# Kernel optimization log

Hardware: AMD Instinct MI355X
Metric: run time of the kernel (lower is better)

## Reference

```python
import jax, jax.numpy as jnp
import numpy as np
import math

B, H, T, DH, D = 1, 8, 2048, 64, 64
NEG_INF = -1e30
EPS = 1e-9

def setup_inputs() -> dict:
    key = jax.random.key(0)
    ks = jax.random.split(key, 6)
    q = jax.random.normal(ks[0], (B, H, T, DH), dtype=jnp.float32)
    k = jax.random.normal(ks[1], (B, H, T, DH), dtype=jnp.float32)
    v = jax.random.normal(ks[2], (B, H, T, DH), dtype=jnp.float32)
    edge_type_bias = 0.1 * jax.random.normal(ks[3], (4,), dtype=jnp.float32)
    neigh_idx = jax.random.randint(ks[4], (H, T, D), 0, T).astype(jnp.int32)
    edge_type = jax.random.randint(ks[5], (H, T, D), 0, 5).astype(jnp.int32)
    return {"q": q, "k": k, "v": v, "edge_type_bias": edge_type_bias,
            "neigh_idx": neigh_idx, "edge_type": edge_type}

def _masked_softmax(scores, mask):
    # scores: [B,H,T,D] fp32, mask: [1,H,T,D] bool; zeros on all-masked rows
    masked = jnp.where(mask, scores, NEG_INF)
    m = jnp.max(masked, axis=-1, keepdims=True)
    e = jnp.where(mask, jnp.exp(masked - m), 0.0)
    denom = jnp.maximum(jnp.sum(e, axis=-1, keepdims=True), EPS)
    return e / denom

def reference(q, k, v, edge_type_bias, neigh_idx, edge_type):
    Bq, Hq, Tq, dh = q.shape
    # safe_neighbor_idx: clamp to valid range
    s_idx = jnp.clip(neigh_idx, 0, Tq - 1)                       # [H,T,D]
    # causal_neighbor_mask: valid (>=0) and neighbor <= query position
    pos = jnp.arange(Tq, dtype=neigh_idx.dtype)[None, :, None]    # [1,T,1]
    mask = (neigh_idx >= 0) & (neigh_idx <= pos)                  # [H,T,D]
    # edge-type bias: type 0 -> no bias, types 1..4 -> learnable bias
    full_bias = jnp.concatenate([jnp.zeros((1,), jnp.float32),
                                 edge_type_bias.astype(jnp.float32)])
    bias_htd = full_bias[edge_type]                               # [H,T,D]
    # gather neighbor K/V: k_g[b,h,t,n,:] = k[b,h,s_idx[h,t,n],:]
    h_ix = jnp.arange(Hq)[:, None, None]                          # [H,1,1]
    k_g = k[:, h_ix, s_idx]                                       # [B,H,T,D,dh]
    v_g = v[:, h_ix, s_idx]                                       # [B,H,T,D,dh]
    scores = jnp.einsum('bhtc,bhtnc->bhtn',
                        q.astype(jnp.float32),
                        k_g.astype(jnp.float32)) / math.sqrt(dh)
    scores = scores + bias_htd[None]                              # [B,H,T,D]
    w = _masked_softmax(scores, mask[None])                       # [B,H,T,D]
    y = jnp.einsum('bhtn,bhtnc->bhtc', w, v_g.astype(jnp.float32))
    return y.astype(v.dtype)
```

## Files before the change

kernel.cpp:

```cpp
#include <hip/hip_runtime.h>
#include <hip/hip_fp16.h>

constexpr int H  = 8;
constexpr int T  = 2048;
constexpr int DH = 64;
constexpr int D  = 64;
constexpr int NKV = H * T * DH;

typedef _Float16 half2v __attribute__((ext_vector_type(2)));

#if defined(__has_builtin)
#if __has_builtin(__builtin_amdgcn_fdot2)
#define HAVE_FDOT2 1
#endif
#if __has_builtin(__builtin_amdgcn_permlane32_swap)
#define HAVE_PL32 1
#endif
#if __has_builtin(__builtin_amdgcn_permlane16_swap)
#define HAVE_PL16 1
#endif
#endif

__device__ __forceinline__ float dot2acc(half2v a, half2v b, float c) {
#ifdef HAVE_FDOT2
    return __builtin_amdgcn_fdot2(a, b, c, false);
#else
    return c + (float)a.x * (float)b.x + (float)a.y * (float)b.y;
#endif
}

__device__ __forceinline__ half2v h2bits(int b) { return __builtin_bit_cast(half2v, b); }

__device__ __forceinline__ half2v f2h2(float x, float y) {
    __half2 h = __float22half2_rn(make_float2(x, y));
    return __builtin_bit_cast(half2v, h);
}

template<int CTRL>
__device__ __forceinline__ float dpp_mov_f(float x) {
    int yi = __builtin_amdgcn_update_dpp(0, __builtin_bit_cast(int, x),
                                         CTRL, 0xF, 0xF, true);
    return __builtin_bit_cast(float, yi);
}
template<int CTRL>
__device__ __forceinline__ float dpp_add_f(float x) { return x + dpp_mov_f<CTRL>(x); }
template<int CTRL>
__device__ __forceinline__ float dpp_max_f(float x) { return fmaxf(x, dpp_mov_f<CTRL>(x)); }

__device__ __forceinline__ float xor32add_f(float x) {
#ifdef HAVE_PL32
    unsigned u = __builtin_bit_cast(unsigned, x);
    auto r = __builtin_amdgcn_permlane32_swap(u, u, false, false);
    return __builtin_bit_cast(float, (unsigned)r[0]) + __builtin_bit_cast(float, (unsigned)r[1]);
#else
    return x + __shfl_xor(x, 32);
#endif
}
__device__ __forceinline__ float xor32max_f(float x) {
#ifdef HAVE_PL32
    unsigned u = __builtin_bit_cast(unsigned, x);
    auto r = __builtin_amdgcn_permlane32_swap(u, u, false, false);
    return fmaxf(__builtin_bit_cast(float, (unsigned)r[0]), __builtin_bit_cast(float, (unsigned)r[1]));
#else
    return fmaxf(x, __shfl_xor(x, 32));
#endif
}
__device__ __forceinline__ float xor16add_f(float x) {
#ifdef HAVE_PL16
    unsigned u = __builtin_bit_cast(unsigned, x);
    auto r = __builtin_amdgcn_permlane16_swap(u, u, false, false);
    return __builtin_bit_cast(float, (unsigned)r[0]) + __builtin_bit_cast(float, (unsigned)r[1]);
#else
    return x + __shfl_xor(x, 16);
#endif
}
__device__ __forceinline__ float xor16max_f(float x) {
#ifdef HAVE_PL16
    unsigned u = __builtin_bit_cast(unsigned, x);
    auto r = __builtin_amdgcn_permlane16_swap(u, u, false, false);
    return fmaxf(__builtin_bit_cast(float, (unsigned)r[0]), __builtin_bit_cast(float, (unsigned)r[1]));
#else
    return fmaxf(x, __shfl_xor(x, 16));
#endif
}
__device__ __forceinline__ half2v xor32add_h2(half2v x) {
#ifdef HAVE_PL32
    unsigned u = __builtin_bit_cast(unsigned, x);
    auto r = __builtin_amdgcn_permlane32_swap(u, u, false, false);
    return h2bits((int)r[0]) + h2bits((int)r[1]);
#else
    return x + h2bits(__shfl_xor(__builtin_bit_cast(int, x), 32));
#endif
}
__device__ __forceinline__ half2v xor16add_h2(half2v x) {
#ifdef HAVE_PL16
    unsigned u = __builtin_bit_cast(unsigned, x);
    auto r = __builtin_amdgcn_permlane16_swap(u, u, false, false);
    return h2bits((int)r[0]) + h2bits((int)r[1]);
#else
    return x + h2bits(__shfl_xor(__builtin_bit_cast(int, x), 16));
#endif
}
__device__ __forceinline__ half2v xor8add_h2(half2v x) {
    return x + h2bits(__shfl_xor(__builtin_bit_cast(int, x), 8));
}

__global__ __launch_bounds__(256) void cvt_f32_f16(
    const float* __restrict__ k, const float* __restrict__ v,
    __half* __restrict__ kh, __half* __restrict__ vh)
{
    const int i = (blockIdx.x * 256 + threadIdx.x) * 8;
    const float* src = (blockIdx.y == 0) ? k : v;
    __half*      dst = (blockIdx.y == 0) ? kh : vh;
    const float4 a = *reinterpret_cast<const float4*>(src + i);
    const float4 b = *reinterpret_cast<const float4*>(src + i + 4);
    __half2 hh[4];
    hh[0] = __float22half2_rn(make_float2(a.x, a.y));
    hh[1] = __float22half2_rn(make_float2(a.z, a.w));
    hh[2] = __float22half2_rn(make_float2(b.x, b.y));
    hh[3] = __float22half2_rn(make_float2(b.z, b.w));
    *reinterpret_cast<float4*>(dst + i) = *reinterpret_cast<const float4*>(hh);
}

__global__ __launch_bounds__(256) void wayfinder_attn_f16(
    const float* __restrict__ q,
    const __half* __restrict__ kh,
    const __half* __restrict__ vh,
    const float* __restrict__ eb,
    const int*   __restrict__ nidx,
    const int*   __restrict__ etyp,
    float* __restrict__ out)
{
    const int wave = threadIdx.x >> 6;
    const int lane = threadIdx.x & 63;
    const int bid  = blockIdx.x;
    const int work = ((bid & 7) << 9) | (bid >> 3);
    const int flat = (work << 2) + wave;
    const int h    = flat >> 11;
    const int t    = flat & (T - 1);
    const int grp  = lane >> 3;
    const int sub  = lane & 7;

    const long long rowoff = (long long)flat * DH;
    const int*      nrow   = nidx + (long long)flat * D;
    const int*      erow   = etyp + (long long)flat * D;

    const int4 i0 = *reinterpret_cast<const int4*>(nrow + grp * 8);
    const int4 i1 = *reinterpret_cast<const int4*>(nrow + grp * 8 + 4);
    const int4 e0 = *reinterpret_cast<const int4*>(erow + grp * 8);
    const int4 e1 = *reinterpret_cast<const int4*>(erow + grp * 8 + 4);

    const float4 qa = *reinterpret_cast<const float4*>(q + rowoff + sub * 8);
    const float4 qb = *reinterpret_cast<const float4*>(q + rowoff + sub * 8 + 4);

    const int idx_i[8] = {i0.x, i0.y, i0.z, i0.w, i1.x, i1.y, i1.z, i1.w};
    const int et_i [8] = {e0.x, e0.y, e0.z, e0.w, e1.x, e1.y, e1.z, e1.w};

    const __half* khead = kh + (long long)h * T * DH;
    const __half* vhead = vh + (long long)h * T * DH;

    int s_i[8];
    int mskbits = 0;
    #pragma unroll
    for (int i = 0; i < 8; ++i) {
        s_i[i] = min(max(idx_i[i], 0), T - 1);
        mskbits |= ((idx_i[i] >= 0) && (idx_i[i] <= t)) ? (1 << i) : 0;
    }

    float4 kf[8], vf[8];
    #pragma unroll
    for (int i = 0; i < 8; ++i) {
        const long long ro = (long long)s_i[i] * DH + sub * 8;
        kf[i] = *reinterpret_cast<const float4*>(khead + ro);
        vf[i] = *reinterpret_cast<const float4*>(vhead + ro);
    }

    const float4 ebv = *reinterpret_cast<const float4*>(eb);
    float bias_i[8];
    #pragma unroll
    for (int i = 0; i < 8; ++i) {
        const int et = et_i[i];
        bias_i[i] = (et == 1) ? ebv.x : (et == 2) ? ebv.y :
                    (et == 3) ? ebv.z : (et == 4) ? ebv.w : 0.0f;
    }

    half2v qp[4];
    qp[0] = f2h2(qa.x, qa.y);
    qp[1] = f2h2(qa.z, qa.w);
    qp[2] = f2h2(qb.x, qb.y);
    qp[3] = f2h2(qb.z, qb.w);

    float sc[8];
    #pragma unroll
    for (int i = 0; i < 8; ++i) {
        const half2v* kp = reinterpret_cast<const half2v*>(&kf[i]);
        float p = dot2acc(qp[0], kp[0],
                  dot2acc(qp[1], kp[1],
                  dot2acc(qp[2], kp[2],
                  dot2acc(qp[3], kp[3], 0.0f))));
        p = dpp_add_f<0xB1>(p);
        p = dpp_add_f<0x4E>(p);
        p = dpp_add_f<0x141>(p);
        sc[i] = p;
    }

    float masked[8];
    float mx = -1e30f;
    #pragma unroll
    for (int i = 0; i < 8; ++i) {
        const bool mk = (mskbits >> i) & 1;
        masked[i] = mk ? fmaf(sc[i], 0.125f, bias_i[i]) : -1e30f;
        mx = fmaxf(mx, masked[i]);
    }
    mx = dpp_max_f<0x140>(mx);
    mx = xor16max_f(mx);
    mx = xor32max_f(mx);

    float e[8];
    float sum = 0.0f;
    #pragma unroll
    for (int i = 0; i < 8; ++i) {
        const bool mk = (mskbits >> i) & 1;
        e[i] = mk ? __expf(masked[i] - mx) : 0.0f;
        sum += e[i];
    }
    sum = dpp_add_f<0x140>(sum);
    sum = xor16add_f(sum);
    sum = xor32add_f(sum);
    const float rden = 1.0f / fmaxf(sum, 1e-9f);

    float acc[8] = {0.f, 0.f, 0.f, 0.f, 0.f, 0.f, 0.f, 0.f};
    #pragma unroll
    for (int i = 0; i < 8; ++i) {
        const float w = e[i] * rden;
        const half2v* vp = reinterpret_cast<const half2v*>(&vf[i]);
        acc[0] += w * (float)vp[0].x;  acc[1] += w * (float)vp[0].y;
        acc[2] += w * (float)vp[1].x;  acc[3] += w * (float)vp[1].y;
        acc[4] += w * (float)vp[2].x;  acc[5] += w * (float)vp[2].y;
        acc[6] += w * (float)vp[3].x;  acc[7] += w * (float)vp[3].y;
    }

    half2v h0 = f2h2(acc[0], acc[1]);
    half2v h1 = f2h2(acc[2], acc[3]);
    half2v h2 = f2h2(acc[4], acc[5]);
    half2v h3 = f2h2(acc[6], acc[7]);
    h0 = xor8add_h2(h0);  h1 = xor8add_h2(h1);
    h2 = xor8add_h2(h2);  h3 = xor8add_h2(h3);
    h0 = xor16add_h2(h0); h1 = xor16add_h2(h1);
    h2 = xor16add_h2(h2); h3 = xor16add_h2(h3);
    h0 = xor32add_h2(h0); h1 = xor32add_h2(h1);
    h2 = xor32add_h2(h2); h3 = xor32add_h2(h3);

    if (lane < 16) {
        const int s8   = (lane & 7) * 8;
        const int half = lane >> 3;
        const float4 o = half
            ? make_float4((float)h2.x, (float)h2.y, (float)h3.x, (float)h3.y)
            : make_float4((float)h0.x, (float)h0.y, (float)h1.x, (float)h1.y);
        *reinterpret_cast<float4*>(out + rowoff + s8 + half * 4) = o;
    }
}

__global__ __launch_bounds__(256) void wayfinder_attn_f32(
    const float* __restrict__ q, const float* __restrict__ k,
    const float* __restrict__ v, const float* __restrict__ eb,
    const int* __restrict__ nidx, const int* __restrict__ etyp,
    float* __restrict__ out)
{
    const int wave = threadIdx.x >> 6;
    const int lane = threadIdx.x & 63;
    const int flat = (blockIdx.x << 2) + wave;
    const int h    = flat >> 11;
    const int t    = flat & (T - 1);
    const int grp  = lane >> 4;
    const int sub  = lane & 15;

    __shared__ int    sidx[4][64];
    __shared__ float  ssc [4][64];
    __shared__ float2 swv [4][64];

    const long long rowoff = (long long)flat * DH;
    const long long noff = (long long)flat * D + lane;
    const int  idx = nidx[noff];
    const int  et  = etyp[noff];
    const int  s   = min(max(idx, 0), T - 1);
    const bool msk = (idx >= 0) && (idx <= t);
    const float4 ebv  = *reinterpret_cast<const float4*>(eb);
    const float  bias = (et == 1) ? ebv.x : (et == 2) ? ebv.y :
                        (et == 3) ? ebv.z : (et == 4) ? ebv.w : 0.0f;
    sidx[wave][lane] = s;
    const float4 qf = *reinterpret_cast<const float4*>(q + rowoff + sub * 4);
    __syncthreads();

    const float* khead = k + (long long)h * T * DH;
    #pragma unroll
    for (int i = 0; i < 16; ++i) {
        const int n  = i * 4 + grp;
        const int sn = sidx[wave][n];
        const float4 kf = *reinterpret_cast<const float4*>(khead + sn * DH + sub * 4);
        float p = qf.x * kf.x + qf.y * kf.y + qf.z * kf.z + qf.w * kf.w;
        p += __shfl_xor(p, 1);
        p += __shfl_xor(p, 2);
        p += __shfl_xor(p, 4);
        p += __shfl_xor(p, 8);
        if (sub == 0) ssc[wave][n] = p;
    }
    __syncthreads();

    const float sc     = ssc[wave][lane];
    const float masked = msk ? (sc * 0.125f + bias) : -1e30f;
    float mx = masked;
    #pragma unroll
    for (int off = 32; off > 0; off >>= 1) mx = fmaxf(mx, __shfl_xor(mx, off));
    const float e = msk ? __expf(masked - mx) : 0.0f;
    float sum = e;
    #pragma unroll
    for (int off = 32; off > 0; off >>= 1) sum += __shfl_xor(sum, off);
    const float w = e / fmaxf(sum, 1e-9f);
    swv[wave][lane] = make_float2(w, __int_as_float(s));
    __syncthreads();

    const float* vhead = v + (long long)h * T * DH;
    float4 acc = make_float4(0.f, 0.f, 0.f, 0.f);
    #pragma unroll
    for (int i = 0; i < 16; ++i) {
        const int    n  = i * 4 + grp;
        const float2 ws = swv[wave][n];
        const int    sn = __float_as_int(ws.y);
        const float4 vf = *reinterpret_cast<const float4*>(vhead + sn * DH + sub * 4);
        acc.x += ws.x * vf.x; acc.y += ws.x * vf.y;
        acc.z += ws.x * vf.z; acc.w += ws.x * vf.w;
    }
    #pragma unroll
    for (int off = 16; off <= 32; off <<= 1) {
        acc.x += __shfl_xor(acc.x, off); acc.y += __shfl_xor(acc.y, off);
        acc.z += __shfl_xor(acc.z, off); acc.w += __shfl_xor(acc.w, off);
    }
    if (lane < 16)
        *reinterpret_cast<float4*>(out + rowoff + sub * 4) = acc;
}

extern "C" void kernel_launch(void* const* d_in, const int* in_sizes, int n_in,
                              void* d_out, int out_size, void* d_ws, size_t ws_size,
                              hipStream_t stream) {
    const float* q    = (const float*)d_in[0];
    const float* k    = (const float*)d_in[1];
    const float* v    = (const float*)d_in[2];
    const float* eb   = (const float*)d_in[3];
    const int*   nidx = (const int*)d_in[4];
    const int*   etyp = (const int*)d_in[5];
    float* out = (float*)d_out;

    const size_t need = (size_t)2 * NKV * sizeof(__half);
    if (ws_size >= need) {
        __half* kh = (__half*)d_ws;
        __half* vh = kh + NKV;
        dim3 cgrid(NKV / (256 * 8), 2);
        hipLaunchKernelGGL(cvt_f32_f16, cgrid, dim3(256), 0, stream, k, v, kh, vh);
        hipLaunchKernelGGL(wayfinder_attn_f16, dim3(H * T / 4), dim3(256), 0, stream,
                           q, kh, vh, eb, nidx, etyp, out);
    } else {
        hipLaunchKernelGGL(wayfinder_attn_f32, dim3(H * T / 4), dim3(256), 0, stream,
                           q, k, v, eb, nidx, etyp, out);
    }
}
```

Measured before the change: 25.32 us.

## Compact causally-valid neighbors via ballot and skip gathers of masked entries

Each wave loads its 64 neighbor indices one per lane, ballots the causal mask, and compacts the valid indices and edge types into a shared-memory buffer using mbcnt prefix positions. The K/V gather, the dot products and the V accumulation then run only for as many 8-wide chunks as there are valid neighbors, which skips memory traffic for masked neighbors (on average about half, given the causal mask on random indices). In exchange it adds an LDS round trip and wave-uniform branching. It also relies on an intra-wave LDS write-then-read with no explicit barrier.

```diff
diff --git a/kernel.cpp b/kernel.cpp
--- a/kernel.cpp
+++ b/kernel.cpp
@@ -18,6 +18,9 @@
 #endif
 #if __has_builtin(__builtin_amdgcn_permlane16_swap)
 #define HAVE_PL16 1
+#endif
+#if __has_builtin(__builtin_amdgcn_mbcnt_lo)
+#define HAVE_MBCNT 1
 #endif
 #endif
 
@@ -131,6 +134,8 @@
     const int*   __restrict__ etyp,
     float* __restrict__ out)
 {
+    __shared__ int cbuf[4][64];
+
     const int wave = threadIdx.x >> 6;
     const int lane = threadIdx.x & 63;
     const int bid  = blockIdx.x;
@@ -142,47 +147,26 @@
     const int sub  = lane & 7;
 
     const long long rowoff = (long long)flat * DH;
-    const int*      nrow   = nidx + (long long)flat * D;
-    const int*      erow   = etyp + (long long)flat * D;
-
-    const int4 i0 = *reinterpret_cast<const int4*>(nrow + grp * 8);
-    const int4 i1 = *reinterpret_cast<const int4*>(nrow + grp * 8 + 4);
-    const int4 e0 = *reinterpret_cast<const int4*>(erow + grp * 8);
-    const int4 e1 = *reinterpret_cast<const int4*>(erow + grp * 8 + 4);
+
+    const int idx = nidx[(long long)flat * D + lane];
+    const int et  = etyp[(long long)flat * D + lane];
+    const bool mk = (unsigned)idx <= (unsigned)t;
+
+    const unsigned long long M = __ballot(mk);
+    const int total = __builtin_amdgcn_readfirstlane((int)__popcll(M));
+#ifdef HAVE_MBCNT
+    const int pos = __builtin_amdgcn_mbcnt_hi((unsigned)(M >> 32),
+                    __builtin_amdgcn_mbcnt_lo((unsigned)M, 0u));
+#else
+    const int pos = (int)__popcll(M & ((1ull << lane) - 1ull));
+#endif
+    if (mk) cbuf[wave][pos] = idx | (et << 11);
 
     const float4 qa = *reinterpret_cast<const float4*>(q + rowoff + sub * 8);
     const float4 qb = *reinterpret_cast<const float4*>(q + rowoff + sub * 8 + 4);
 
-    const int idx_i[8] = {i0.x, i0.y, i0.z, i0.w, i1.x, i1.y, i1.z, i1.w};
-    const int et_i [8] = {e0.x, e0.y, e0.z, e0.w, e1.x, e1.y, e1.z, e1.w};
-
     const __half* khead = kh + (long long)h * T * DH;
     const __half* vhead = vh + (long long)h * T * DH;
-
-    int s_i[8];
-    int mskbits = 0;
-    #pragma unroll
-    for (int i = 0; i < 8; ++i) {
-        s_i[i] = min(max(idx_i[i], 0), T - 1);
-        mskbits |= ((idx_i[i] >= 0) && (idx_i[i] <= t)) ? (1 << i) : 0;
-    }
-
-    float4 kf[8], vf[8];
-    #pragma unroll
-    for (int i = 0; i < 8; ++i) {
-        const long long ro = (long long)s_i[i] * DH + sub * 8;
-        kf[i] = *reinterpret_cast<const float4*>(khead + ro);
-        vf[i] = *reinterpret_cast<const float4*>(vhead + ro);
-    }
-
-    const float4 ebv = *reinterpret_cast<const float4*>(eb);
-    float bias_i[8];
-    #pragma unroll
-    for (int i = 0; i < 8; ++i) {
-        const int et = et_i[i];
-        bias_i[i] = (et == 1) ? ebv.x : (et == 2) ? ebv.y :
-                    (et == 3) ? ebv.z : (et == 4) ? ebv.w : 0.0f;
-    }
 
     half2v qp[4];
     qp[0] = f2h2(qa.x, qa.y);
@@ -190,27 +174,48 @@
     qp[2] = f2h2(qb.x, qb.y);
     qp[3] = f2h2(qb.z, qb.w);
 
-    float sc[8];
-    #pragma unroll
-    for (int i = 0; i < 8; ++i) {
-        const half2v* kp = reinterpret_cast<const half2v*>(&kf[i]);
-        float p = dot2acc(qp[0], kp[0],
-                  dot2acc(qp[1], kp[1],
-                  dot2acc(qp[2], kp[2],
-                  dot2acc(qp[3], kp[3], 0.0f))));
-        p = dpp_add_f<0xB1>(p);
-        p = dpp_add_f<0x4E>(p);
-        p = dpp_add_f<0x141>(p);
-        sc[i] = p;
+    int packed[8] = {0, 0, 0, 0, 0, 0, 0, 0};
+    float4 kf[8], vf[8];
+    #pragma unroll
+    for (int j = 0; j < 8; ++j) {
+        if (total > j * 8) {
+            const int c  = min(j * 8 + grp, total - 1);
+            const int pk = cbuf[wave][c];
+            packed[j] = pk;
+            const long long ro = (long long)(pk & 0x7FF) * DH + sub * 8;
+            kf[j] = *reinterpret_cast<const float4*>(khead + ro);
+            vf[j] = *reinterpret_cast<const float4*>(vhead + ro);
+        }
+    }
+
+    const float4 ebv = *reinterpret_cast<const float4*>(eb);
+
+    float sc[8] = {0.f, 0.f, 0.f, 0.f, 0.f, 0.f, 0.f, 0.f};
+    #pragma unroll
+    for (int j = 0; j < 8; ++j) {
+        if (total > j * 8) {
+            const half2v* kp = reinterpret_cast<const half2v*>(&kf[j]);
+            float p = dot2acc(qp[0], kp[0],
+                      dot2acc(qp[1], kp[1],
+                      dot2acc(qp[2], kp[2],
+                      dot2acc(qp[3], kp[3], 0.0f))));
+            p = dpp_add_f<0xB1>(p);
+            p = dpp_add_f<0x4E>(p);
+            p = dpp_add_f<0x141>(p);
+            sc[j] = p;
+        }
     }
 
     float masked[8];
     float mx = -1e30f;
     #pragma unroll
-    for (int i = 0; i < 8; ++i) {
-        const bool mk = (mskbits >> i) & 1;
-        masked[i] = mk ? fmaf(sc[i], 0.125f, bias_i[i]) : -1e30f;
-        mx = fmaxf(mx, masked[i]);
+    for (int j = 0; j < 8; ++j) {
+        const bool valid = (j * 8 + grp) < total;
+        const int  etj   = packed[j] >> 11;
+        const float bias = (etj == 1) ? ebv.x : (etj == 2) ? ebv.y :
+                           (etj == 3) ? ebv.z : (etj == 4) ? ebv.w : 0.0f;
+        masked[j] = valid ? fmaf(sc[j], 0.125f, bias) : -1e30f;
+        mx = fmaxf(mx, masked[j]);
     }
     mx = dpp_max_f<0x140>(mx);
     mx = xor16max_f(mx);
@@ -219,10 +224,10 @@
     float e[8];
     float sum = 0.0f;
     #pragma unroll
-    for (int i = 0; i < 8; ++i) {
-        const bool mk = (mskbits >> i) & 1;
-        e[i] = mk ? __expf(masked[i] - mx) : 0.0f;
-        sum += e[i];
+    for (int j = 0; j < 8; ++j) {
+        const bool valid = (j * 8 + grp) < total;
+        e[j] = valid ? __expf(masked[j] - mx) : 0.0f;
+        sum += e[j];
     }
     sum = dpp_add_f<0x140>(sum);
     sum = xor16add_f(sum);
@@ -231,13 +236,15 @@
 
     float acc[8] = {0.f, 0.f, 0.f, 0.f, 0.f, 0.f, 0.f, 0.f};
     #pragma unroll
-    for (int i = 0; i < 8; ++i) {
-        const float w = e[i] * rden;
-        const half2v* vp = reinterpret_cast<const half2v*>(&vf[i]);
-        acc[0] += w * (float)vp[0].x;  acc[1] += w * (float)vp[0].y;
-        acc[2] += w * (float)vp[1].x;  acc[3] += w * (float)vp[1].y;
-        acc[4] += w * (float)vp[2].x;  acc[5] += w * (float)vp[2].y;
-        acc[6] += w * (float)vp[3].x;  acc[7] += w * (float)vp[3].y;
+    for (int j = 0; j < 8; ++j) {
+        if (total > j * 8) {
+            const float w = e[j] * rden;
+            const half2v* vp = reinterpret_cast<const half2v*>(&vf[j]);
+            acc[0] += w * (float)vp[0].x;  acc[1] += w * (float)vp[0].y;
+            acc[2] += w * (float)vp[1].x;  acc[3] += w * (float)vp[1].y;
+            acc[4] += w * (float)vp[2].x;  acc[5] += w * (float)vp[2].y;
+            acc[6] += w * (float)vp[3].x;  acc[7] += w * (float)vp[3].y;
+        }
     }
 
     half2v h0 = f2h2(acc[0], acc[1]);
```

Result: slower. 34.18 us (+35.0%).
